# Kernel optimization log

Hardware: AMD Instinct MI355X
Metric: run time of the kernel (lower is better)

## Reference

```python
import jax, jax.numpy as jnp
import numpy as np
import math

B, C, L_SEQ, PRED = 32, 21, 512, 96
D, H, DFF, NLAYERS = 512, 8, 2048, 3
E = D // H
PATCH_LEN, STRIDE, PAD = 16, 8, 8
PATCH_NUM = (L_SEQ - PATCH_LEN) // STRIDE + 2  # 64
MA = 25          # moving-average kernel of series_decomp
FACTOR = 1
TOP_K = int(FACTOR * math.log(PATCH_NUM))  # top-k delays in AutoCorrelation


def _pos_embedding(max_len, d_model):
    pos = np.arange(max_len, dtype=np.float32)[:, None]
    div = np.exp(np.arange(0, d_model, 2, dtype=np.float32) * -(math.log(10000.0) / d_model))
    pe = np.zeros((max_len, d_model), np.float32)
    pe[:, 0::2] = np.sin(pos * div)
    pe[:, 1::2] = np.cos(pos * div)
    return jnp.asarray(pe)

POS_EMB = _pos_embedding(PATCH_NUM, D)


def setup_inputs():
    key = jax.random.key(0)
    ks = iter(jax.random.split(key, 48))
    g = lambda shape, s=0.02: jax.random.normal(next(ks), shape, jnp.float32) * s
    inp = {"x_enc": jax.random.normal(next(ks), (B, L_SEQ, C), jnp.float32)}
    inp["w_val"] = g((PATCH_LEN, D))  # PatchEmbedding value_embedding (no bias)
    for tag in ("ac", "sa"):
        for nm in ("Wq", "Wk", "Wv", "Wo"):
            inp[nm + "_" + tag] = g((NLAYERS, D, D))
        for nm in ("bq", "bk", "bv", "bo"):
            inp[nm + "_" + tag] = g((NLAYERS, D))
    inp["Wf"] = g((NLAYERS, 2 * D, D))
    inp["bf"] = g((NLAYERS, D))
    inp["W1"] = g((NLAYERS, D, DFF))   # conv1 (1x1, no bias)
    inp["W2"] = g((NLAYERS, DFF, D))   # conv2 (1x1, no bias)
    inp["bn_g"] = jnp.ones((D,), jnp.float32)
    inp["bn_b"] = jnp.zeros((D,), jnp.float32)
    inp["W_head"] = g((D * PATCH_NUM, PRED))
    inp["b_head"] = g((PRED,))
    return inp


def _proj_heads(x, W, b):
    N, L, _ = x.shape
    return (x @ W + b).reshape(N, L, H, E)


def _auto_corr(x, Wq, bq, Wk, bk, Wv, bv, Wo, bo):
    # AutoCorrelation (training-mode time_delay_agg): FFT correlation + top-k roll aggregation
    N, L, _ = x.shape
    q = _proj_heads(x, Wq, bq)
    k = _proj_heads(x, Wk, bk)
    v = _proj_heads(x, Wv, bv)
    qf = jnp.fft.rfft(q.transpose(0, 2, 3, 1), axis=-1)   # [N,H,E,Lf]
    kf = jnp.fft.rfft(k.transpose(0, 2, 3, 1), axis=-1)
    corr = jnp.fft.irfft(qf * jnp.conj(kf), n=L, axis=-1)  # [N,H,E,L]
    vals = v.transpose(0, 2, 3, 1)                          # [N,H,E,L]
    mean_corr = corr.mean(axis=(1, 2))                      # [N,L]
    _, top_idx = jax.lax.top_k(mean_corr.mean(axis=0), TOP_K)  # delays shared across batch
    w = jax.nn.softmax(mean_corr[:, top_idx], axis=-1)      # [N,TOP_K]
    rolled = jax.vmap(lambda s: jnp.roll(vals, -s, axis=-1))(top_idx)  # [K,N,H,E,L]
    agg = jnp.einsum('knhel,nk->nhel', rolled, w)
    return agg.transpose(0, 3, 1, 2).reshape(N, L, D) @ Wo + bo


def _full_attn(x, Wq, bq, Wk, bk, Wv, bv, Wo, bo):
    N, L, _ = x.shape
    q = _proj_heads(x, Wq, bq)
    k = _proj_heads(x, Wk, bk)
    v = _proj_heads(x, Wv, bv)
    scores = jnp.einsum('blhe,bshe->bhls', q, k) / math.sqrt(E)
    out = jnp.einsum('bhls,bshe->blhe', jax.nn.softmax(scores, axis=-1), v)
    return out.reshape(N, L, D) @ Wo + bo


def _decomp(x):
    # series_decomp: residual after edge-replicated moving average (returns seasonal part)
    half = (MA - 1) // 2
    xp = jnp.concatenate([jnp.repeat(x[:, :1], half, axis=1), x,
                          jnp.repeat(x[:, -1:], half, axis=1)], axis=1)
    cs = jnp.cumsum(xp, axis=1)
    cs = jnp.concatenate([jnp.zeros_like(cs[:, :1]), cs], axis=1)
    mean = (cs[:, MA:] - cs[:, :-MA]) / MA
    return x - mean


def _forward(x_enc, w_val, Wq_ac, bq_ac, Wk_ac, bk_ac, Wv_ac, bv_ac, Wo_ac, bo_ac,
             Wq_sa, bq_sa, Wk_sa, bk_sa, Wv_sa, bv_sa, Wo_sa, bo_sa,
             Wf, bf, W1, W2, bn_g, bn_b, W_head, b_head):
    # instance normalization over time
    means = x_enc.mean(axis=1, keepdims=True)                 # [B,1,C]
    xc = x_enc - means
    stdev = jnp.sqrt(xc.var(axis=1, keepdims=True) + 1e-5)    # [B,1,C]
    xn = xc / stdev
    # patch embedding (channel independent): replication-pad end, unfold, linear + pos emb
    xp = xn.transpose(0, 2, 1)                                # [B,C,L]
    xp = jnp.concatenate([xp, jnp.repeat(xp[..., -1:], PAD, axis=-1)], axis=-1)
    idx = jnp.arange(PATCH_NUM)[:, None] * STRIDE + jnp.arange(PATCH_LEN)[None, :]
    patches = xp[..., idx]                                    # [B,C,P,patch_len]
    x = patches.reshape(B * C, PATCH_NUM, PATCH_LEN) @ w_val + POS_EMB  # [B*C,P,D]
    # hybrid encoder layers
    for l in range(NLAYERS):
        a = _auto_corr(x, Wq_ac[l], bq_ac[l], Wk_ac[l], bk_ac[l], Wv_ac[l], bv_ac[l], Wo_ac[l], bo_ac[l])
        s = _full_attn(x, Wq_sa[l], bq_sa[l], Wk_sa[l], bk_sa[l], Wv_sa[l], bv_sa[l], Wo_sa[l], bo_sa[l])
        fused = jnp.concatenate([a, s], axis=-1) @ Wf[l] + bf[l]
        x = _decomp(x + fused)
        y = jax.nn.relu(x @ W1[l]) @ W2[l]                    # 1x1 convs == pointwise linears
        x = _decomp(x + y)
    # final BatchNorm1d over d_model channels (batch statistics, affine)
    mu = x.mean(axis=(0, 1))
    var = x.var(axis=(0, 1))
    x = (x - mu) / jnp.sqrt(var + 1e-5) * bn_g + bn_b
    # head: [B*C,P,D] -> [B,C,D,P] -> flat (d-major) -> pred_len
    enc = x.reshape(B, C, PATCH_NUM, D).transpose(0, 1, 3, 2).reshape(B, C, D * PATCH_NUM)
    dec = (enc @ W_head + b_head).transpose(0, 2, 1)          # [B,PRED,C]
    return dec * stdev[:, 0][:, None, :] + means[:, 0][:, None, :]


def reference(x_enc, w_val, Wq_ac, bq_ac, Wk_ac, bk_ac, Wv_ac, bv_ac, Wo_ac, bo_ac,
              Wq_sa, bq_sa, Wk_sa, bk_sa, Wv_sa, bv_sa, Wo_sa, bo_sa,
              Wf, bf, W1, W2, bn_g, bn_b, W_head, b_head):
    return _forward(x_enc, w_val, Wq_ac, bq_ac, Wk_ac, bk_ac, Wv_ac, bv_ac, Wo_ac, bo_ac,
                    Wq_sa, bq_sa, Wk_sa, bk_sa, Wv_sa, bv_sa, Wo_sa, bo_sa,
                    Wf, bf, W1, W2, bn_g, bn_b, W_head, b_head)
```

## Files before the change

### kernel.cpp

```cpp
#include <hip/hip_runtime.h>
#include <math.h>


typedef unsigned short u16;
typedef short s16x8 __attribute__((ext_vector_type(8)));
typedef u16 u16x8 __attribute__((ext_vector_type(8)));
typedef float f32x4 __attribute__((ext_vector_type(4)));

#define MROWS 43008
#define NSEQ  672

__device__ __forceinline__ float bf2f(u16 b) {
  union { unsigned u; float f; } v; v.u = ((unsigned)b) << 16; return v.f;
}
__device__ __forceinline__ u16 f2bf(float f) {
  union { float f; unsigned u; } v; v.f = f;
  unsigned r = v.u + 0x7FFFu + ((v.u >> 16) & 1u);
  return (u16)(r >> 16);
}

__device__ __forceinline__ void gload16(const u16* g, u16* l) {
  __builtin_amdgcn_global_load_lds(
      (const __attribute__((address_space(1))) unsigned int*)g,
      (__attribute__((address_space(3))) unsigned int*)l, 16, 0, 0);
}

__global__ __launch_bounds__(256) void zero_out_kernel(float* __restrict__ o, int n) {
  int i = blockIdx.x * 256 + threadIdx.x;
  if (i < n) o[i] = 0.f;
}

__global__ __launch_bounds__(256) void transpose_cvt_b(
    const float* __restrict__ W, u16* __restrict__ Wt, int K, int N,
    long long sW, long long sT) {
  __shared__ float t[32][33];
  int z = blockIdx.z;
  W += (size_t)z * sW;
  Wt += (size_t)z * sT;
  int k0 = blockIdx.x * 32, n0 = blockIdx.y * 32;
  int tx = threadIdx.x, ty = threadIdx.y;
#pragma unroll
  for (int i = 0; i < 32; i += 8)
    t[ty + i][tx] = W[(size_t)(k0 + ty + i) * N + n0 + tx];
  __syncthreads();
#pragma unroll
  for (int i = 0; i < 32; i += 8)
    Wt[(size_t)(n0 + ty + i) * K + k0 + tx] = f2bf(t[tx][ty + i]);
}

__global__ __launch_bounds__(256) void transpose_cvt_six(
    const float* __restrict__ Wq_sa, const float* __restrict__ Wk_sa,
    const float* __restrict__ Wv_sa, const float* __restrict__ Wq_ac,
    const float* __restrict__ Wk_ac, const float* __restrict__ Wv_ac,
    u16* __restrict__ dst) {
  __shared__ float t[32][33];
  int z = blockIdx.z;
  int l = z / 6, wi = z % 6;
  const float* srcs[6] = {Wq_sa, Wk_sa, Wv_sa, Wq_ac, Wk_ac, Wv_ac};
  const float* W = srcs[wi] + (size_t)l * 262144;
  u16* out = dst + ((size_t)l * 6 + wi) * 262144;
  int k0 = blockIdx.x * 32, n0 = blockIdx.y * 32;
  int tx = threadIdx.x, ty = threadIdx.y;
#pragma unroll
  for (int i = 0; i < 32; i += 8)
    t[ty + i][tx] = W[(size_t)(k0 + ty + i) * 512 + n0 + tx];
  __syncthreads();
#pragma unroll
  for (int i = 0; i < 32; i += 8)
    out[(size_t)(n0 + ty + i) * 512 + k0 + tx] = f2bf(t[tx][ty + i]);
}

__global__ __launch_bounds__(256) void cvt_bf16_nine(
    const float* __restrict__ Wo_ac, const float* __restrict__ Wo_sa,
    const float* __restrict__ Wv_ac, u16* __restrict__ dst) {
  int z = blockIdx.z;
  int l = z / 3, s = z % 3;
  const float* base = (s == 0) ? Wo_ac : (s == 1 ? Wo_sa : Wv_ac);
  const float* src = base + (size_t)l * 262144;
  u16* out = dst + ((size_t)l * 3 + s) * 262144;
  int i = blockIdx.x * 256 + threadIdx.x;
  if (i < 262144) out[i] = f2bf(src[i]);
}

__global__ __launch_bounds__(512) void boa_eff_kernel(
    const float* __restrict__ Wo_ac, const float* __restrict__ bo_ac,
    const float* __restrict__ bv_ac, float* __restrict__ out) {
  int l = blockIdx.x;
  int i = threadIdx.x;
  const float* Wo = Wo_ac + (size_t)l * 262144;
  float s = bo_ac[l * 512 + i];
  for (int k = 0; k < 512; k++) s += bv_ac[l * 512 + k] * Wo[(size_t)k * 512 + i];
  out[l * 512 + i] = s;
}

__global__ __launch_bounds__(512) void bias_combine(
    const float* __restrict__ WfW, const float* __restrict__ bfW,
    const float* __restrict__ boa_eff, const float* __restrict__ bo_sa,
    float* __restrict__ out) {
  int l = blockIdx.x;
  const float* Wf = WfW + (size_t)l * 524288;
  int n = threadIdx.x;
  float s = bfW[l * 512 + n];
  for (int i = 0; i < 512; i++) s += boa_eff[l * 512 + i] * Wf[(size_t)i * 512 + n];
  for (int i = 0; i < 512; i++) s += bo_sa[l * 512 + i] * Wf[(size_t)(512 + i) * 512 + n];
  out[l * 512 + n] = s;
}

__global__ __launch_bounds__(512, 4) void gemm128x256(
    const u16* __restrict__ A1, const u16* __restrict__ A2, int lda, int ksplit,
    const u16* __restrict__ Bt, int ldb,
    const float* __restrict__ b0, const float* __restrict__ b1,
    const float* __restrict__ b2,
    u16* __restrict__ C, int ldc, int K, int relu, int nb) {
  __shared__ u16 smA[3][128 * 32];
  __shared__ u16 smB[3][256 * 32];
  int g = blockIdx.x;
  if ((gridDim.x & 7) == 0) g = (g & 7) * (gridDim.x >> 3) + (g >> 3);
  int m0 = (g / nb) * 128, n0 = (g % nb) * 256;
  int tid = threadIdx.x, lane = tid & 63, wid = tid >> 6;
  int wr = wid >> 2, wc = wid & 3;
  int m_in = lane & 15, kq = lane >> 4;
  int sr = tid >> 2;
  int gsl = (((tid & 3) ^ ((sr >> 1) & 3)) * 8);

  int offA[4], offB[4];
#pragma unroll
  for (int mf = 0; mf < 4; mf++) {
    int row = wr * 64 + mf * 16 + m_in;
    offA[mf] = row * 32 + ((kq ^ ((row >> 1) & 3)) * 8);
  }
#pragma unroll
  for (int nf = 0; nf < 4; nf++) {
    int row = wc * 64 + nf * 16 + m_in;
    offB[nf] = row * 32 + ((kq ^ ((row >> 1) & 3)) * 8);
  }
  f32x4 acc[4][4];
#pragma unroll
  for (int i = 0; i < 4; i++)
#pragma unroll
    for (int j = 0; j < 4; j++) acc[i][j] = (f32x4){0.f, 0.f, 0.f, 0.f};

  int nt = K >> 5;
  auto STAGE = [&](int b, int t) {
    int k0 = t * 32;
    const u16* Ap; int kk;
    if (k0 < ksplit) { Ap = A1; kk = k0; } else { Ap = A2; kk = k0 - ksplit; }
    gload16(&Ap[(size_t)(m0 + sr) * lda + kk + gsl], &smA[b][wid * 512]);
    gload16(&Bt[(size_t)(n0 + sr) * ldb + k0 + gsl], &smB[b][wid * 512]);
    gload16(&Bt[(size_t)(n0 + 128 + sr) * ldb + k0 + gsl],
            &smB[b][4096 + wid * 512]);
  };

  STAGE(0, 0);
  STAGE(1, 1 < nt ? 1 : nt - 1);
  int cb = 0;
  for (int t = 0; t < nt; ++t) {
    int pf = t + 2 < nt ? t + 2 : nt - 1;
    int pb = cb + 2 >= 3 ? cb - 1 : cb + 2;
    STAGE(pb, pf);
    asm volatile("s_waitcnt vmcnt(6)" ::: "memory");
    asm volatile("s_barrier" ::: "memory");
    const u16* la = &smA[cb][0];
    const u16* lb = &smB[cb][0];
    s16x8 a_[4], b_[4];
#pragma unroll
    for (int mf = 0; mf < 4; mf++) a_[mf] = *(const s16x8*)&la[offA[mf]];
#pragma unroll
    for (int nf = 0; nf < 4; nf++) b_[nf] = *(const s16x8*)&lb[offB[nf]];
    __builtin_amdgcn_s_setprio(1);
#pragma unroll
    for (int mf = 0; mf < 4; mf++)
#pragma unroll
      for (int nf = 0; nf < 4; nf++)
        acc[mf][nf] = __builtin_amdgcn_mfma_f32_16x16x32_bf16(
            a_[mf], b_[nf], acc[mf][nf], 0, 0, 0);
    __builtin_amdgcn_s_setprio(0);
    asm volatile("s_barrier" ::: "memory");
    cb = cb + 1 >= 3 ? 0 : cb + 1;
  }
  int r0 = m0 + wr * 64 + (kq << 2);
#pragma unroll
  for (int mf = 0; mf < 4; mf++) {
#pragma unroll
    for (int nf = 0; nf < 4; nf++) {
      int col = n0 + wc * 64 + nf * 16 + m_in;
      const float* bp = (col < 512) ? b0 : (col < 1024 ? b1 : b2);
      float bv = bp ? bp[col & 511] : 0.f;
#pragma unroll
      for (int r = 0; r < 4; r++) {
        float v = acc[mf][nf][r] + bv;
        if (relu) v = fmaxf(v, 0.f);
        C[(size_t)(r0 + mf * 16 + r) * ldc + col] = f2bf(v);
      }
    }
  }
}

__global__ __launch_bounds__(256) void gemm128p(
    const u16* __restrict__ A1, const u16* __restrict__ A2, int lda, int ksplit,
    const u16* __restrict__ Bt, int ldb,
    const float* __restrict__ b0, const float* __restrict__ b1,
    const float* __restrict__ b2,
    u16* __restrict__ C, int ldc, int K, int relu, int nb,
    long long syA, long long syB, long long syC) {
  __shared__ u16 sm[3][8192];
  int zy = blockIdx.y;
  A1 += (size_t)zy * syA;
  A2 += (size_t)zy * syA;
  Bt += (size_t)zy * syB;
  C  += (size_t)zy * syC;
  int g = blockIdx.x;
  if ((gridDim.x & 7) == 0) g = (g & 7) * (gridDim.x >> 3) + (g >> 3);
  int m0 = (g / nb) * 128, n0 = (g % nb) * 128;
  int tid = threadIdx.x, lane = tid & 63, w = tid >> 6;
  int wr = w >> 1, wc = w & 1;
  int srow = w * 16 + (lane >> 2);
  int scol = (((lane & 3) ^ ((lane >> 3) & 3)) * 8);
  int m_in = lane & 15;
  int sgrp = lane >> 4;
  int offA[4], offB[4];
#pragma unroll
  for (int mf = 0; mf < 4; mf++) {
    int row = wr * 64 + mf * 16 + m_in;
    offA[mf] = row * 32 + ((sgrp ^ ((row >> 1) & 3)) * 8);
  }
#pragma unroll
  for (int nf = 0; nf < 4; nf++) {
    int row = wc * 64 + nf * 16 + m_in;
    offB[nf] = 4096 + row * 32 + ((sgrp ^ ((row >> 1) & 3)) * 8);
  }
  f32x4 acc[4][4];
#pragma unroll
  for (int i = 0; i < 4; i++)
#pragma unroll
    for (int j = 0; j < 4; j++) acc[i][j] = (f32x4){0.f, 0.f, 0.f, 0.f};

  int nt = K >> 5;
  auto STAGE = [&](int b, int t) {
    int k0 = t * 32;
    const u16* Ab; int kk;
    if (k0 < ksplit) { Ab = A1; kk = k0; } else { Ab = A2; kk = k0 - ksplit; }
    u16* base = &sm[b][0];
    gload16(&Ab[(size_t)(m0 + srow) * lda + kk + scol],      base + w * 512);
    gload16(&Ab[(size_t)(m0 + 64 + srow) * lda + kk + scol], base + 2048 + w * 512);
    gload16(&Bt[(size_t)(n0 + srow) * ldb + k0 + scol],      base + 4096 + w * 512);
    gload16(&Bt[(size_t)(n0 + 64 + srow) * ldb + k0 + scol], base + 6144 + w * 512);
  };

  STAGE(0, 0);
  STAGE(1, 1 < nt ? 1 : nt - 1);
  int cb = 0;
  for (int t = 0; t < nt; ++t) {
    int pf = t + 2 < nt ? t + 2 : nt - 1;
    int pb = cb + 2 >= 3 ? cb - 1 : cb + 2;
    STAGE(pb, pf);
    asm volatile("s_waitcnt vmcnt(8)" ::: "memory");
    asm volatile("s_barrier" ::: "memory");
    const u16* lb = &sm[cb][0];
    s16x8 a_[4], b_[4];
#pragma unroll
    for (int mf = 0; mf < 4; mf++) a_[mf] = *(const s16x8*)&lb[offA[mf]];
#pragma unroll
    for (int nf = 0; nf < 4; nf++) b_[nf] = *(const s16x8*)&lb[offB[nf]];
    __builtin_amdgcn_s_setprio(1);
#pragma unroll
    for (int mf = 0; mf < 4; mf++)
#pragma unroll
      for (int nf = 0; nf < 4; nf++)
        acc[mf][nf] = __builtin_amdgcn_mfma_f32_16x16x32_bf16(
            a_[mf], b_[nf], acc[mf][nf], 0, 0, 0);
    __builtin_amdgcn_s_setprio(0);
    asm volatile("s_barrier" ::: "memory");
    cb = cb + 1 >= 3 ? 0 : cb + 1;
  }
  int r0 = m0 + wr * 64 + (sgrp << 2);
  int cl = lane & 15;
#pragma unroll
  for (int mf = 0; mf < 4; mf++) {
#pragma unroll
    for (int nf = 0; nf < 4; nf++) {
      int col = n0 + wc * 64 + nf * 16 + cl;
      const float* bp = (col < 512) ? b0 : (col < 1024 ? b1 : b2);
      float bv = bp ? bp[col & 511] : 0.f;
#pragma unroll
      for (int r = 0; r < 4; r++) {
        float v = acc[mf][nf][r] + bv;
        if (relu) v = fmaxf(v, 0.f);
        C[(size_t)(r0 + mf * 16 + r) * ldc + col] = f2bf(v);
      }
    }
  }
}

__global__ __launch_bounds__(256) void gram_mc_kernel(
    const u16* __restrict__ Q, const u16* __restrict__ K, int ld,
    float* __restrict__ MC) {
  __shared__ u16 lA[64][40];
  __shared__ u16 lB[64][40];
  __shared__ float red[64];
  int n = blockIdx.x;
  int tid = threadIdx.x, lane = tid & 63, w = tid >> 6;
  int sr = tid >> 2, scol = (tid & 3) * 8;
  if (tid < 64) red[tid] = 0.f;
  f32x4 acc[4];
#pragma unroll
  for (int i = 0; i < 4; i++) acc[i] = (f32x4){0.f, 0.f, 0.f, 0.f};
  size_t base = (size_t)n * 64 * ld;
  for (int k0 = 0; k0 < 512; k0 += 32) {
    *(u16x8*)&lA[sr][scol] = *(const u16x8*)&Q[base + (size_t)sr * ld + k0 + scol];
    *(u16x8*)&lB[sr][scol] = *(const u16x8*)&K[base + (size_t)sr * ld + k0 + scol];
    __syncthreads();
    int ar = w * 16 + (lane & 15);
    int kk = (lane >> 4) * 8;
    s16x8 af = *(const s16x8*)&lA[ar][kk];
#pragma unroll
    for (int nb = 0; nb < 4; nb++) {
      s16x8 bfr = *(const s16x8*)&lB[nb * 16 + (lane & 15)][kk];
      acc[nb] = __builtin_amdgcn_mfma_f32_16x16x32_bf16(af, bfr, acc[nb], 0, 0, 0);
    }
    __syncthreads();
  }
  int row0 = w * 16 + ((lane >> 4) << 2);
  int cl = lane & 15;
#pragma unroll
  for (int nb = 0; nb < 4; nb++) {
    int col = nb * 16 + cl;
#pragma unroll
    for (int r = 0; r < 4; r++)
      atomicAdd(&red[(row0 + r - col) & 63], acc[nb][r]);
  }
  __syncthreads();
  if (tid < 64) MC[n * 64 + tid] = red[tid] * (1.f / 512.f);
}

__global__ __launch_bounds__(256) void instnorm_kernel(
    const float* __restrict__ xe, float* __restrict__ MEANS, float* __restrict__ STDEV) {
  int n = blockIdx.x;
  int b = n / 21, c = n % 21;
  int tid = threadIdx.x;
  float v0 = xe[((size_t)b * 512 + tid) * 21 + c];
  float v1 = xe[((size_t)b * 512 + tid + 256) * 21 + c];
  float s = v0 + v1, ss = v0 * v0 + v1 * v1;
  for (int o = 32; o; o >>= 1) { s += __shfl_down(s, o); ss += __shfl_down(ss, o); }
  __shared__ float rs[4], rss[4];
  if ((tid & 63) == 0) { rs[tid >> 6] = s; rss[tid >> 6] = ss; }
  __syncthreads();
  if (tid == 0) {
    s = rs[0] + rs[1] + rs[2] + rs[3];
    ss = rss[0] + rss[1] + rss[2] + rss[3];
    float mean = s * (1.f / 512.f);
    float var = ss * (1.f / 512.f) - mean * mean;
    MEANS[n] = mean;
    STDEV[n] = sqrtf(var + 1e-5f);
  }
}

__global__ __launch_bounds__(256) void pe_kernel(float* __restrict__ PE) {
  int i = blockIdx.x * 256 + threadIdx.x;
  int p = i >> 9, d = i & 511;
  int k = d >> 1;
  float freq = expf(-(float)(2 * k) * (9.210340371976184f / 512.f));
  float ang = (float)p * freq;
  PE[i] = (d & 1) ? cosf(ang) : sinf(ang);
}

__global__ __launch_bounds__(256) void patch_kernel(
    const float* __restrict__ xe, const float* __restrict__ wv,
    const float* __restrict__ PE, const float* __restrict__ MEANS,
    const float* __restrict__ STDEV, u16* __restrict__ X) {
  __shared__ float pw[16][512];
  __shared__ float pat[8][16];
  int bx = blockIdx.x;
  int n = bx >> 3, pb = bx & 7;
  int b = n / 21, c = n % 21;
  int tid = threadIdx.x;
  float mean = MEANS[n], inv = 1.f / STDEV[n];
  for (int i = tid; i < 8192; i += 256) pw[i >> 9][i & 511] = wv[i];
  if (tid < 128) {
    int pp = tid >> 4, j = tid & 15;
    int l = (pb * 8 + pp) * 8 + j;
    if (l > 511) l = 511;
    pat[pp][j] = (xe[((size_t)b * 512 + l) * 21 + c] - mean) * inv;
  }
  __syncthreads();
  for (int i = tid; i < 4096; i += 256) {
    int pp = i >> 9, d = i & 511;
    int p = pb * 8 + pp;
    float s = PE[p * 512 + d];
#pragma unroll
    for (int j = 0; j < 16; j++) s += pat[pp][j] * pw[j][d];
    X[((size_t)n * 64 + p) * 512 + d] = f2bf(s);
  }
}

__global__ __launch_bounds__(256) void topk_softw_kernel(
    const float* __restrict__ MC, int* __restrict__ TIDX, float* __restrict__ WSM) {
  __shared__ float g[256];
  __shared__ float gt[64];
  __shared__ int dly[4];
  int tid = threadIdx.x;
  int tau = tid & 63, part = tid >> 6;
  float s = 0.f;
  for (int n = part * 168; n < (part + 1) * 168; n++) s += MC[n * 64 + tau];
  g[tid] = s;
  __syncthreads();
  if (tid < 64) gt[tid] = g[tid] + g[64 + tid] + g[128 + tid] + g[192 + tid];
  __syncthreads();
  if (tid == 0) {
    for (int j = 0; j < 4; j++) {
      int best = 0; float bv = -1e30f;
      for (int t = 0; t < 64; t++) if (gt[t] > bv) { bv = gt[t]; best = t; }
      dly[j] = best;
      TIDX[j] = best;
      gt[best] = -1e30f;
    }
  }
  __syncthreads();
  for (int n = tid; n < 672; n += 256) {
    float v[4], mx = -1e30f;
#pragma unroll
    for (int j = 0; j < 4; j++) { v[j] = MC[n * 64 + dly[j]]; mx = fmaxf(mx, v[j]); }
    float ssum = 0.f;
#pragma unroll
    for (int j = 0; j < 4; j++) { v[j] = __expf(v[j] - mx); ssum += v[j]; }
    float inv = 1.f / ssum;
#pragma unroll
    for (int j = 0; j < 4; j++) WSM[n * 4 + j] = v[j] * inv;
  }
}

__global__ __launch_bounds__(256) void agg_kernel(
    const u16* __restrict__ V, int ldv, const float* __restrict__ WSM,
    const int* __restrict__ TIDX, u16* __restrict__ OUT, int ldo) {
  int n = blockIdx.x;
  __shared__ float w[4];
  __shared__ int dly[4];
  int tid = threadIdx.x;
  if (tid < 4) { w[tid] = WSM[n * 4 + tid]; dly[tid] = TIDX[tid]; }
  __syncthreads();
  for (int i = tid; i < 64 * 512; i += 256) {
    int l = i >> 9, d = i & 511;
    float s = 0.f;
#pragma unroll
    for (int j = 0; j < 4; j++)
      s += w[j] * bf2f(V[((size_t)n * 64 + ((l + dly[j]) & 63)) * ldv + d]);
    OUT[((size_t)n * 64 + l) * ldo + d] = f2bf(s);
  }
}

__global__ __launch_bounds__(256) void attn_mfma(u16* __restrict__ QKV) {
  __shared__ u16 lq[64][72], lk[64][72], lvt[64][72], lp[64][72];
  int n = blockIdx.x >> 3, h = blockIdx.x & 7;
  size_t base = (size_t)n * 64 * 1536;
  int qo = h * 64, ko = 512 + h * 64, vo = 1024 + h * 64;
  int tid = threadIdx.x, lane = tid & 63, w = tid >> 6;
  int r = tid >> 2, c0 = (tid & 3) * 16;
  *(u16x8*)&lq[r][c0]     = *(const u16x8*)&QKV[base + (size_t)r * 1536 + qo + c0];
  *(u16x8*)&lq[r][c0 + 8] = *(const u16x8*)&QKV[base + (size_t)r * 1536 + qo + c0 + 8];
  *(u16x8*)&lk[r][c0]     = *(const u16x8*)&QKV[base + (size_t)r * 1536 + ko + c0];
  *(u16x8*)&lk[r][c0 + 8] = *(const u16x8*)&QKV[base + (size_t)r * 1536 + ko + c0 + 8];
  u16x8 v0 = *(const u16x8*)&QKV[base + (size_t)r * 1536 + vo + c0];
  u16x8 v1 = *(const u16x8*)&QKV[base + (size_t)r * 1536 + vo + c0 + 8];
#pragma unroll
  for (int j = 0; j < 8; j++) { lvt[c0 + j][r] = v0[j]; lvt[c0 + 8 + j][r] = v1[j]; }
  __syncthreads();
  int m_in = lane & 15, ks = (lane >> 4) * 8;
  int rq = lane >> 4;
  s16x8 aq0 = *(const s16x8*)&lq[w * 16 + m_in][ks];
  s16x8 aq1 = *(const s16x8*)&lq[w * 16 + m_in][32 + ks];
  f32x4 s4[4];
#pragma unroll
  for (int nf = 0; nf < 4; nf++) {
    s4[nf] = (f32x4){0.f, 0.f, 0.f, 0.f};
    s16x8 b0 = *(const s16x8*)&lk[nf * 16 + m_in][ks];
    s16x8 b1 = *(const s16x8*)&lk[nf * 16 + m_in][32 + ks];
    s4[nf] = __builtin_amdgcn_mfma_f32_16x16x32_bf16(aq0, b0, s4[nf], 0, 0, 0);
    s4[nf] = __builtin_amdgcn_mfma_f32_16x16x32_bf16(aq1, b1, s4[nf], 0, 0, 0);
  }
  float mx[4] = {-1e30f, -1e30f, -1e30f, -1e30f};
#pragma unroll
  for (int nf = 0; nf < 4; nf++)
#pragma unroll
    for (int r4 = 0; r4 < 4; r4++) {
      s4[nf][r4] *= 0.125f;
      mx[r4] = fmaxf(mx[r4], s4[nf][r4]);
    }
#pragma unroll
  for (int o = 1; o < 16; o <<= 1)
#pragma unroll
    for (int r4 = 0; r4 < 4; r4++) mx[r4] = fmaxf(mx[r4], __shfl_xor(mx[r4], o));
  float sum[4] = {0.f, 0.f, 0.f, 0.f};
#pragma unroll
  for (int nf = 0; nf < 4; nf++)
#pragma unroll
    for (int r4 = 0; r4 < 4; r4++) {
      float e = __expf(s4[nf][r4] - mx[r4]);
      s4[nf][r4] = e;
      sum[r4] += e;
    }
#pragma unroll
  for (int o = 1; o < 16; o <<= 1)
#pragma unroll
    for (int r4 = 0; r4 < 4; r4++) sum[r4] += __shfl_xor(sum[r4], o);
#pragma unroll
  for (int nf = 0; nf < 4; nf++)
#pragma unroll
    for (int r4 = 0; r4 < 4; r4++)
      lp[w * 16 + rq * 4 + r4][nf * 16 + m_in] = f2bf(s4[nf][r4] / sum[r4]);
  __syncthreads();
  s16x8 ap0 = *(const s16x8*)&lp[w * 16 + m_in][ks];
  s16x8 ap1 = *(const s16x8*)&lp[w * 16 + m_in][32 + ks];
#pragma unroll
  for (int nf = 0; nf < 4; nf++) {
    f32x4 o4 = (f32x4){0.f, 0.f, 0.f, 0.f};
    s16x8 b0 = *(const s16x8*)&lvt[nf * 16 + m_in][ks];
    s16x8 b1 = *(const s16x8*)&lvt[nf * 16 + m_in][32 + ks];
    o4 = __builtin_amdgcn_mfma_f32_16x16x32_bf16(ap0, b0, o4, 0, 0, 0);
    o4 = __builtin_amdgcn_mfma_f32_16x16x32_bf16(ap1, b1, o4, 0, 0, 0);
#pragma unroll
    for (int r4 = 0; r4 < 4; r4++)
      QKV[base + (size_t)(w * 16 + rq * 4 + r4) * 1536 + qo + nf * 16 + m_in] =
          f2bf(o4[r4]);
  }
}

__global__ __launch_bounds__(256) void decomp_kernel(
    u16* __restrict__ X, const u16* __restrict__ DELTA, int ds) {
  int n = blockIdx.x >> 1;
  int d = ((blockIdx.x & 1) << 8) + threadIdx.x;
  size_t xb = ((size_t)n * 64) * 512 + d;
  size_t db = ((size_t)n * 64) * ds + d;
  float v[64];
#pragma unroll
  for (int l = 0; l < 64; l++)
    v[l] = bf2f(X[xb + (size_t)l * 512]) + bf2f(DELTA[db + (size_t)l * ds]);
  float s = 12.f * v[0];
#pragma unroll
  for (int t = 0; t <= 12; t++) s += v[t];
#pragma unroll
  for (int l = 0; l < 64; l++) {
    float out = v[l] - s * (1.f / 25.f);
    X[xb + (size_t)l * 512] = f2bf(out);
    if (l < 63) {
      int add = l + 13; if (add > 63) add = 63;
      int sub = l - 12; if (sub < 0) sub = 0;
      s += v[add] - v[sub];
    }
  }
}

__global__ __launch_bounds__(256) void bn_part(
    const u16* __restrict__ X, float* __restrict__ PS) {
  int ch = blockIdx.x, tid = threadIdx.x;
  float s1a = 0, s2a = 0, s1b = 0, s2b = 0;
  size_t base = (size_t)ch * 128 * 512;
  for (int r = 0; r < 128; r++) {
    float a = bf2f(X[base + (size_t)r * 512 + tid]);
    float b = bf2f(X[base + (size_t)r * 512 + tid + 256]);
    s1a += a; s2a += a * a; s1b += b; s2b += b * b;
  }
  PS[(size_t)(ch * 2 + 0) * 512 + tid] = s1a;
  PS[(size_t)(ch * 2 + 0) * 512 + tid + 256] = s1b;
  PS[(size_t)(ch * 2 + 1) * 512 + tid] = s2a;
  PS[(size_t)(ch * 2 + 1) * 512 + tid + 256] = s2b;
}

__global__ __launch_bounds__(256) void bn_final(
    const float* __restrict__ PS, const float* __restrict__ g,
    const float* __restrict__ b, float* __restrict__ SCALE, float* __restrict__ SHIFT) {
  int d = blockIdx.x * 256 + threadIdx.x;
  float s = 0, ss = 0;
  for (int c = 0; c < 336; c++) {
    s += PS[(size_t)(c * 2) * 512 + d];
    ss += PS[(size_t)(c * 2 + 1) * 512 + d];
  }
  float mu = s * (1.f / 43008.f);
  float var = ss * (1.f / 43008.f) - mu * mu;
  float inv = 1.f / sqrtf(var + 1e-5f);
  float sc = g[d] * inv;
  SCALE[d] = sc;
  SHIFT[d] = b[d] - mu * sc;
}

__global__ __launch_bounds__(256) void bn_transpose_kernel(
    const u16* __restrict__ X, const float* __restrict__ SCALE,
    const float* __restrict__ SHIFT, u16* __restrict__ ENC) {
  __shared__ u16 t[64][72];
  int n = blockIdx.x >> 3, dc = (blockIdx.x & 7) * 64;
  int tid = threadIdx.x;
  for (int i = tid; i < 4096; i += 256) {
    int p = i >> 6, d = i & 63;
    float v = bf2f(X[((size_t)n * 64 + p) * 512 + dc + d]) * SCALE[dc + d] + SHIFT[dc + d];
    t[p][d] = f2bf(v);
  }
  __syncthreads();
  for (int i = tid; i < 4096; i += 256) {
    int d = i >> 6, p = i & 63;
    ENC[(size_t)n * 32768 + (size_t)(dc + d) * 64 + p] = t[p][d];
  }
}

__global__ __launch_bounds__(256) void head_gemm(
    const u16* __restrict__ ENC, const u16* __restrict__ Wht,
    float* __restrict__ PART) {
  __shared__ u16 lA[64][40];
  __shared__ u16 lB[96][40];
  int bm = blockIdx.x;
  int kc = blockIdx.y;
  int tid = threadIdx.x, lane = tid & 63, w = tid >> 6;
  int sr = tid >> 2, sc0 = (tid & 3) * 8;
  f32x4 acc[6];
#pragma unroll
  for (int i = 0; i < 6; i++) acc[i] = (f32x4){0.f, 0.f, 0.f, 0.f};
  for (int kk0 = 0; kk0 < 2048; kk0 += 32) {
    int k0 = kc * 2048 + kk0;
    *(u16x8*)&lA[sr][sc0] =
        *(const u16x8*)&ENC[(size_t)(bm * 64 + sr) * 32768 + k0 + sc0];
    for (int i = tid; i < 96 * 4; i += 256) {
      int rB = i >> 2, seg = (i & 3) * 8;
      *(u16x8*)&lB[rB][seg] = *(const u16x8*)&Wht[(size_t)rB * 32768 + k0 + seg];
    }
    __syncthreads();
    int ar = w * 16 + (lane & 15);
    int kk = (lane >> 4) * 8;
    s16x8 af = *(const s16x8*)&lA[ar][kk];
#pragma unroll
    for (int nb = 0; nb < 6; nb++) {
      s16x8 bfr = *(const s16x8*)&lB[nb * 16 + (lane & 15)][kk];
      acc[nb] = __builtin_amdgcn_mfma_f32_16x16x32_bf16(af, bfr, acc[nb], 0, 0, 0);
    }
    __syncthreads();
  }
  int rb = bm * 64 + w * 16 + ((lane >> 4) << 2);
  int cl = lane & 15;
#pragma unroll
  for (int nb = 0; nb < 6; nb++) {
    int col = nb * 16 + cl;
#pragma unroll
    for (int r = 0; r < 4; r++) {
      int row = rb + r;
      if (row < 672) PART[((size_t)kc * 672 + row) * 96 + col] = acc[nb][r];
    }
  }
}

__global__ __launch_bounds__(256) void head_reduce(
    const float* __restrict__ PART, const float* __restrict__ bh,
    const float* __restrict__ STDEV, const float* __restrict__ MEANS,
    float* __restrict__ OUT) {
  int i = blockIdx.x * 256 + threadIdx.x;
  if (i >= 672 * 96) return;
  int n = i / 96, r = i % 96;
  float s = bh[r];
  for (int kc = 0; kc < 16; kc++) s += PART[((size_t)kc * 672 + n) * 96 + r];
  int b = n / 21, c = n % 21;
  OUT[((size_t)b * 96 + r) * 21 + c] = s * STDEV[n] + MEANS[n];
}

extern "C" void kernel_launch(void* const* d_in, const int* in_sizes, int n_in,
                              void* d_out, int out_size, void* d_ws, size_t ws_size,
                              hipStream_t stream) {
  const float* x_enc = (const float*)d_in[0];
  const float* w_val = (const float*)d_in[1];
  const float* Wq_ac = (const float*)d_in[2];
  const float* Wk_ac = (const float*)d_in[3];
  const float* Wv_ac = (const float*)d_in[4];
  const float* Wo_ac = (const float*)d_in[5];
  const float* bq_ac = (const float*)d_in[6];
  const float* bk_ac = (const float*)d_in[7];
  const float* bv_ac = (const float*)d_in[8];
  const float* bo_ac = (const float*)d_in[9];
  const float* Wq_sa = (const float*)d_in[10];
  const float* Wk_sa = (const float*)d_in[11];
  const float* Wv_sa = (const float*)d_in[12];
  const float* Wo_sa = (const float*)d_in[13];
  const float* bq_sa = (const float*)d_in[14];
  const float* bk_sa = (const float*)d_in[15];
  const float* bv_sa = (const float*)d_in[16];
  const float* bo_sa = (const float*)d_in[17];
  const float* WfW   = (const float*)d_in[18];
  const float* bfW   = (const float*)d_in[19];
  const float* W1    = (const float*)d_in[20];
  const float* W2    = (const float*)d_in[21];
  const float* bn_g  = (const float*)d_in[22];
  const float* bn_b  = (const float*)d_in[23];
  const float* W_head = (const float*)d_in[24];
  const float* b_head = (const float*)d_in[25];
  (void)in_sizes; (void)n_in; (void)out_size;

  char* wsp = (char*)d_ws;
  size_t off = 0;
  auto alloc = [&](size_t bytes) -> void* {
    void* p = wsp + off;
    off += (bytes + 255) & ~(size_t)255;
    return p;
  };
  u16* X    = (u16*)alloc((size_t)MROWS * 512 * 2);
  u16* Q3   = (u16*)alloc((size_t)MROWS * 1536 * 2);
  u16* SIX   = (u16*)alloc((size_t)3 * 6 * 262144 * 2);
  u16* W1T   = (u16*)alloc((size_t)3 * 1048576 * 2);
  u16* W2T   = (u16*)alloc((size_t)3 * 1048576 * 2);
  u16* WFT   = (u16*)alloc((size_t)3 * 524288 * 2);
  u16* WORIG = (u16*)alloc((size_t)3 * 3 * 262144 * 2);
  u16* WCOMB = (u16*)alloc((size_t)3 * 524288 * 2);
  u16* WHT   = (u16*)alloc((size_t)3145728 * 2);
  u16* TMP   = (u16*)alloc((size_t)3 * 262144 * 2);
  float* PE = (float*)alloc((size_t)32768 * 4);
  float* MEANS = (float*)alloc(672 * 4);
  float* STDEV = (float*)alloc(672 * 4);
  float* MC = (float*)alloc(672 * 64 * 4);
  int* TIDX = (int*)alloc(4 * 4);
  float* WSM = (float*)alloc(672 * 4 * 4);
  float* BNP = (float*)alloc((size_t)336 * 1024 * 4);
  float* SCALE = (float*)alloc(512 * 4);
  float* SHIFT = (float*)alloc(512 * 4);
  float* BOAE = (float*)alloc(3 * 512 * 4);
  float* BCOMB = (float*)alloc(3 * 512 * 4);
  u16* C0 = Q3;
  u16* C1 = Q3 + 512;
  u16* C2 = Q3 + 1024;
  u16* HBUF = Q3;
  u16* YBUF = Q3 + (size_t)21504 * 2048;
  u16* ENC  = Q3;
  float* HEADP = (float*)X;

  if (off > ws_size) {
    zero_out_kernel<<<252, 256, 0, stream>>>((float*)d_out, 672 * 96);
    return;
  }

  transpose_cvt_six<<<dim3(16, 16, 18), dim3(32, 8), 0, stream>>>(
      Wq_sa, Wk_sa, Wv_sa, Wq_ac, Wk_ac, Wv_ac, SIX);
  transpose_cvt_b<<<dim3(16, 64, 3), dim3(32, 8), 0, stream>>>(
      W1, W1T, 512, 2048, 1048576, 1048576);
  transpose_cvt_b<<<dim3(64, 16, 3), dim3(32, 8), 0, stream>>>(
      W2, W2T, 2048, 512, 1048576, 1048576);
  transpose_cvt_b<<<dim3(32, 16, 3), dim3(32, 8), 0, stream>>>(
      WfW, WFT, 1024, 512, 524288, 524288);
  transpose_cvt_b<<<dim3(1024, 3, 1), dim3(32, 8), 0, stream>>>(
      W_head, WHT, 32768, 96, 0, 0);
  cvt_bf16_nine<<<dim3(1024, 1, 9), 256, 0, stream>>>(Wo_ac, Wo_sa, Wv_ac, WORIG);
  boa_eff_kernel<<<3, 512, 0, stream>>>(Wo_ac, bo_ac, bv_ac, BOAE);
  bias_combine<<<3, 512, 0, stream>>>(WfW, bfW, BOAE, bo_sa, BCOMB);
  gemm128p<<<dim3(16, 3), 256, 0, stream>>>(
      WFT, WFT, 1024, 512, WORIG, 512, nullptr, nullptr, nullptr,
      TMP, 512, 512, 0, 4, 524288, 3 * 262144, 262144);
  gemm128p<<<dim3(16, 3), 256, 0, stream>>>(
      TMP, TMP, 512, 512, WORIG + 2 * 262144, 512, nullptr, nullptr, nullptr,
      WCOMB, 1024, 512, 0, 4, 262144, 3 * 262144, 524288);
  gemm128p<<<dim3(16, 3), 256, 0, stream>>>(
      WFT + 512, WFT + 512, 1024, 512, WORIG + 262144, 512,
      nullptr, nullptr, nullptr, WCOMB + 512, 1024, 512, 0, 4,
      524288, 3 * 262144, 524288);

  instnorm_kernel<<<672, 256, 0, stream>>>(x_enc, MEANS, STDEV);
  pe_kernel<<<128, 256, 0, stream>>>(PE);
  patch_kernel<<<672 * 8, 256, 0, stream>>>(x_enc, w_val, PE, MEANS, STDEV, X);

  auto gbig = [&](const u16* A1, const u16* A2, int lda, int ksplit,
                  const u16* Bt, int ldb, const float* b0, const float* b1,
                  const float* b2, u16* C, int ldc, int M, int N, int K,
                  int relu) {
    int nb = N / 256;
    if (nb < 1) nb = 1;
    gemm128x256<<<(M / 128) * nb, 512, 0, stream>>>(
        A1, A2, lda, ksplit, Bt, ldb, b0, b1, b2, C, ldc, K, relu, nb);
  };

  for (int l = 0; l < 3; l++) {
    const u16* qkv_sa = SIX + (size_t)l * 6 * 262144;
    const u16* qk_ac  = qkv_sa + (size_t)3 * 262144;
    const u16* w1     = W1T + (size_t)l * 1048576;
    const u16* w2     = W2T + (size_t)l * 1048576;
    const u16* wcomb  = WCOMB + (size_t)l * 524288;
    gbig(X, X, 512, 512, qkv_sa, 512, bq_sa + l * 512, bk_sa + l * 512,
         bv_sa + l * 512, Q3, 1536, MROWS, 1536, 512, 0);
    attn_mfma<<<5376, 256, 0, stream>>>(Q3);
    gbig(X, X, 512, 512, qk_ac, 512, bq_ac + l * 512, bk_ac + l * 512, nullptr,
         C1, 1536, MROWS, 1024, 512, 0);
    gram_mc_kernel<<<672, 256, 0, stream>>>(C1, C2, 1536, MC);
    topk_softw_kernel<<<1, 256, 0, stream>>>(MC, TIDX, WSM);
    agg_kernel<<<672, 256, 0, stream>>>(X, 512, WSM, TIDX, C2, 1536);
    gbig(C2, C0, 1536, 512, wcomb, 1024, BCOMB + l * 512, nullptr, nullptr,
         C1, 1536, MROWS, 512, 1024, 0);
    decomp_kernel<<<1344, 256, 0, stream>>>(X, C1, 1536);
    for (int c = 0; c < 2; c++) {
      const u16* Xc = X + (size_t)c * 21504 * 512;
      u16* Yc = YBUF + (size_t)c * 21504 * 512;
      gbig(Xc, Xc, 512, 512, w1, 512, nullptr, nullptr, nullptr,
           HBUF, 2048, 21504, 2048, 512, 1);
      gemm128x256<<<(21504 / 128) * 2, 512, 0, stream>>>(
          HBUF, HBUF, 2048, 2048, w2, 2048, nullptr, nullptr, nullptr,
          Yc, 512, 2048, 0, 2);
    }
    decomp_kernel<<<1344, 256, 0, stream>>>(X, YBUF, 512);
  }

  bn_part<<<336, 256, 0, stream>>>(X, BNP);
  bn_final<<<2, 256, 0, stream>>>(BNP, bn_g, bn_b, SCALE, SHIFT);
  bn_transpose_kernel<<<672 * 8, 256, 0, stream>>>(X, SCALE, SHIFT, ENC);
  head_gemm<<<dim3(11, 16), 256, 0, stream>>>(ENC, WHT, HEADP);
  head_reduce<<<252, 256, 0, stream>>>(HEADP, b_head, STDEV, MEANS, (float*)d_out);
}
```

Before: 2.224 ms.

## Fold AutoCorrelation Q/K projections into one precombined Wq·Wkᵀ weight

After: 2.160 ms, median of 2. 2.9% less time.

```diff
diff --git a/kernel.cpp b/kernel.cpp
--- a/kernel.cpp
+++ b/kernel.cpp
@@ -48,17 +48,15 @@
     Wt[(size_t)(n0 + ty + i) * K + k0 + tx] = f2bf(t[tx][ty + i]);
 }
 
-__global__ __launch_bounds__(256) void transpose_cvt_six(
+__global__ __launch_bounds__(256) void transpose_cvt_sa(
     const float* __restrict__ Wq_sa, const float* __restrict__ Wk_sa,
-    const float* __restrict__ Wv_sa, const float* __restrict__ Wq_ac,
-    const float* __restrict__ Wk_ac, const float* __restrict__ Wv_ac,
-    u16* __restrict__ dst) {
+    const float* __restrict__ Wv_sa, u16* __restrict__ dst) {
   __shared__ float t[32][33];
   int z = blockIdx.z;
-  int l = z / 6, wi = z % 6;
-  const float* srcs[6] = {Wq_sa, Wk_sa, Wv_sa, Wq_ac, Wk_ac, Wv_ac};
+  int l = z / 3, wi = z % 3;
+  const float* srcs[3] = {Wq_sa, Wk_sa, Wv_sa};
   const float* W = srcs[wi] + (size_t)l * 262144;
-  u16* out = dst + ((size_t)l * 6 + wi) * 262144;
+  u16* out = dst + ((size_t)l * 3 + wi) * 262144;
   int k0 = blockIdx.x * 32, n0 = blockIdx.y * 32;
   int tx = threadIdx.x, ty = threadIdx.y;
 #pragma unroll
@@ -70,14 +68,15 @@
     out[(size_t)(n0 + ty + i) * 512 + k0 + tx] = f2bf(t[tx][ty + i]);
 }
 
-__global__ __launch_bounds__(256) void cvt_bf16_nine(
+__global__ __launch_bounds__(256) void cvt_bf16_fifteen(
     const float* __restrict__ Wo_ac, const float* __restrict__ Wo_sa,
-    const float* __restrict__ Wv_ac, u16* __restrict__ dst) {
+    const float* __restrict__ Wv_ac, const float* __restrict__ Wq_ac,
+    const float* __restrict__ Wk_ac, u16* __restrict__ dst) {
   int z = blockIdx.z;
-  int l = z / 3, s = z % 3;
-  const float* base = (s == 0) ? Wo_ac : (s == 1 ? Wo_sa : Wv_ac);
-  const float* src = base + (size_t)l * 262144;
-  u16* out = dst + ((size_t)l * 3 + s) * 262144;
+  int l = z / 5, s = z % 5;
+  const float* bases[5] = {Wo_ac, Wo_sa, Wv_ac, Wq_ac, Wk_ac};
+  const float* src = bases[s] + (size_t)l * 262144;
+  u16* out = dst + ((size_t)l * 5 + s) * 262144;
   int i = blockIdx.x * 256 + threadIdx.x;
   if (i < 262144) out[i] = f2bf(src[i]);
 }
@@ -293,7 +292,7 @@
 }
 
 __global__ __launch_bounds__(256) void gram_mc_kernel(
-    const u16* __restrict__ Q, const u16* __restrict__ K, int ld,
+    const u16* __restrict__ Q, int ldq, const u16* __restrict__ K, int ldk,
     float* __restrict__ MC) {
   __shared__ u16 lA[64][40];
   __shared__ u16 lB[64][40];
@@ -305,10 +304,11 @@
   f32x4 acc[4];
 #pragma unroll
   for (int i = 0; i < 4; i++) acc[i] = (f32x4){0.f, 0.f, 0.f, 0.f};
-  size_t base = (size_t)n * 64 * ld;
+  size_t bq = (size_t)n * 64 * ldq;
+  size_t bk = (size_t)n * 64 * ldk;
   for (int k0 = 0; k0 < 512; k0 += 32) {
-    *(u16x8*)&lA[sr][scol] = *(const u16x8*)&Q[base + (size_t)sr * ld + k0 + scol];
-    *(u16x8*)&lB[sr][scol] = *(const u16x8*)&K[base + (size_t)sr * ld + k0 + scol];
+    *(u16x8*)&lA[sr][scol] = *(const u16x8*)&Q[bq + (size_t)sr * ldq + k0 + scol];
+    *(u16x8*)&lB[sr][scol] = *(const u16x8*)&K[bk + (size_t)sr * ldk + k0 + scol];
     __syncthreads();
     int ar = w * 16 + (lane & 15);
     int kk = (lane >> 4) * 8;
@@ -687,6 +687,7 @@
   const float* W_head = (const float*)d_in[24];
   const float* b_head = (const float*)d_in[25];
   (void)in_sizes; (void)n_in; (void)out_size;
+  (void)bq_ac; (void)bk_ac;
 
   char* wsp = (char*)d_ws;
   size_t off = 0;
@@ -697,12 +698,13 @@
   };
   u16* X    = (u16*)alloc((size_t)MROWS * 512 * 2);
   u16* Q3   = (u16*)alloc((size_t)MROWS * 1536 * 2);
-  u16* SIX   = (u16*)alloc((size_t)3 * 6 * 262144 * 2);
+  u16* SIX   = (u16*)alloc((size_t)3 * 3 * 262144 * 2);
   u16* W1T   = (u16*)alloc((size_t)3 * 1048576 * 2);
   u16* W2T   = (u16*)alloc((size_t)3 * 1048576 * 2);
   u16* WFT   = (u16*)alloc((size_t)3 * 524288 * 2);
-  u16* WORIG = (u16*)alloc((size_t)3 * 3 * 262144 * 2);
+  u16* WORIG = (u16*)alloc((size_t)3 * 5 * 262144 * 2);
   u16* WCOMB = (u16*)alloc((size_t)3 * 524288 * 2);
+  u16* WQKT  = (u16*)alloc((size_t)3 * 262144 * 2);
   u16* WHT   = (u16*)alloc((size_t)3145728 * 2);
   u16* TMP   = (u16*)alloc((size_t)3 * 262144 * 2);
   float* PE = (float*)alloc((size_t)32768 * 4);
@@ -729,8 +731,8 @@
     return;
   }
 
-  transpose_cvt_six<<<dim3(16, 16, 18), dim3(32, 8), 0, stream>>>(
-      Wq_sa, Wk_sa, Wv_sa, Wq_ac, Wk_ac, Wv_ac, SIX);
+  transpose_cvt_sa<<<dim3(16, 16, 9), dim3(32, 8), 0, stream>>>(
+      Wq_sa, Wk_sa, Wv_sa, SIX);
   transpose_cvt_b<<<dim3(16, 64, 3), dim3(32, 8), 0, stream>>>(
       W1, W1T, 512, 2048, 1048576, 1048576);
   transpose_cvt_b<<<dim3(64, 16, 3), dim3(32, 8), 0, stream>>>(
@@ -739,19 +741,24 @@
       WfW, WFT, 1024, 512, 524288, 524288);
   transpose_cvt_b<<<dim3(1024, 3, 1), dim3(32, 8), 0, stream>>>(
       W_head, WHT, 32768, 96, 0, 0);
-  cvt_bf16_nine<<<dim3(1024, 1, 9), 256, 0, stream>>>(Wo_ac, Wo_sa, Wv_ac, WORIG);
+  cvt_bf16_fifteen<<<dim3(1024, 1, 15), 256, 0, stream>>>(
+      Wo_ac, Wo_sa, Wv_ac, Wq_ac, Wk_ac, WORIG);
   boa_eff_kernel<<<3, 512, 0, stream>>>(Wo_ac, bo_ac, bv_ac, BOAE);
   bias_combine<<<3, 512, 0, stream>>>(WfW, bfW, BOAE, bo_sa, BCOMB);
   gemm128p<<<dim3(16, 3), 256, 0, stream>>>(
       WFT, WFT, 1024, 512, WORIG, 512, nullptr, nullptr, nullptr,
-      TMP, 512, 512, 0, 4, 524288, 3 * 262144, 262144);
+      TMP, 512, 512, 0, 4, 524288, 5 * 262144, 262144);
   gemm128p<<<dim3(16, 3), 256, 0, stream>>>(
       TMP, TMP, 512, 512, WORIG + 2 * 262144, 512, nullptr, nullptr, nullptr,
-      WCOMB, 1024, 512, 0, 4, 262144, 3 * 262144, 524288);
+      WCOMB, 1024, 512, 0, 4, 262144, 5 * 262144, 524288);
   gemm128p<<<dim3(16, 3), 256, 0, stream>>>(
       WFT + 512, WFT + 512, 1024, 512, WORIG + 262144, 512,
       nullptr, nullptr, nullptr, WCOMB + 512, 1024, 512, 0, 4,
-      524288, 3 * 262144, 524288);
+      524288, 5 * 262144, 524288);
+  gemm128p<<<dim3(16, 3), 256, 0, stream>>>(
+      WORIG + 4 * 262144, WORIG + 4 * 262144, 512, 512,
+      WORIG + 3 * 262144, 512, nullptr, nullptr, nullptr,
+      WQKT, 512, 512, 0, 4, 5 * 262144, 5 * 262144, 262144);
 
   instnorm_kernel<<<672, 256, 0, stream>>>(x_enc, MEANS, STDEV);
   pe_kernel<<<128, 256, 0, stream>>>(PE);
@@ -768,17 +775,17 @@
   };
 
   for (int l = 0; l < 3; l++) {
-    const u16* qkv_sa = SIX + (size_t)l * 6 * 262144;
-    const u16* qk_ac  = qkv_sa + (size_t)3 * 262144;
+    const u16* qkv_sa = SIX + (size_t)l * 3 * 262144;
+    const u16* wqkt   = WQKT + (size_t)l * 262144;
     const u16* w1     = W1T + (size_t)l * 1048576;
     const u16* w2     = W2T + (size_t)l * 1048576;
     const u16* wcomb  = WCOMB + (size_t)l * 524288;
     gbig(X, X, 512, 512, qkv_sa, 512, bq_sa + l * 512, bk_sa + l * 512,
          bv_sa + l * 512, Q3, 1536, MROWS, 1536, 512, 0);
     attn_mfma<<<5376, 256, 0, stream>>>(Q3);
-    gbig(X, X, 512, 512, qk_ac, 512, bq_ac + l * 512, bk_ac + l * 512, nullptr,
-         C1, 1536, MROWS, 1024, 512, 0);
-    gram_mc_kernel<<<672, 256, 0, stream>>>(C1, C2, 1536, MC);
+    gbig(X, X, 512, 512, wqkt, 512, nullptr, nullptr, nullptr,
+         C1, 1536, MROWS, 512, 512, 0);
+    gram_mc_kernel<<<672, 256, 0, stream>>>(C1, 1536, X, 512, MC);
     topk_softw_kernel<<<1, 256, 0, stream>>>(MC, TIDX, WSM);
     agg_kernel<<<672, 256, 0, stream>>>(X, 512, WSM, TIDX, C2, 1536);
     gbig(C2, C0, 1536, 512, wcomb, 1024, BCOMB + l * 512, nullptr, nullptr,
```
